# Optimization experiments

Measured on AMD Instinct MI355X. Metric: run time of the kernel, lower is better.

Reference implementation:

```python
import jax, jax.numpy as jnp
import numpy as np

BETA = 0.25


def setup_inputs() -> dict:
    key = jax.random.key(0)
    k1, k2 = jax.random.split(key)
    inputs = jax.random.normal(k1, (32, 4096, 64), dtype=jnp.float32)
    # VarianceScaling(uniform) ~ small-magnitude init; plain normal scaled works for a numeric reference
    codebook = jax.random.normal(k2, (1024, 64), dtype=jnp.float32) * (1.0 / np.sqrt(64.0))
    return {"inputs": inputs, "codebook": codebook}


def reference(inputs, codebook):
    D = codebook.shape[-1]
    flat = jnp.reshape(inputs, (-1, D))                      # [N, D]
    flat_sqr = jnp.sum(flat ** 2, axis=-1, keepdims=True)    # [N, 1]
    code_sqr = jnp.sum(codebook ** 2, axis=-1)[None, :]      # [1, K]
    # full pairwise squared distances [N, K]
    distances = flat_sqr - 2.0 * (flat @ codebook.T) + code_sqr
    encoding_indices = jnp.reshape(jnp.argmin(distances, axis=-1), inputs.shape[:-1])
    quantize = codebook[encoding_indices]                    # gather -> [..., D]
    encoding_loss = jnp.mean((jax.lax.stop_gradient(inputs) - quantize) ** 2)
    commit_loss = jnp.mean((inputs - jax.lax.stop_gradient(quantize)) ** 2)
    loss = encoding_loss + BETA * commit_loss
    # straight-through estimator
    z_q = inputs + jax.lax.stop_gradient(quantize - inputs)
    return loss, z_q, encoding_indices
```

## Files before the change

### kernel.cpp

```cpp
#include <hip/hip_runtime.h>

#define N_ROWS 131072
#define D 64
#define K_CODES 1024
#define RPB 128
#define CH_TILES 4
#define NCHUNK 16

typedef _Float16 f16x8 __attribute__((ext_vector_type(8)));
typedef float    f32x4 __attribute__((ext_vector_type(4)));

#define MFMA16(a, b, c) __builtin_amdgcn_mfma_f32_16x16x32_f16((a), (b), (c), 0, 0, 0)

#define ASYNC_COPY16(gp, lp)                                                  \
    __builtin_amdgcn_global_load_lds(                                         \
        (const __attribute__((address_space(1))) void*)(gp),                  \
        (__attribute__((address_space(3))) void*)(lp), 16, 0, 0)

__global__ __launch_bounds__(256)
void prep_kernel(const float* __restrict__ CB, _Float16* __restrict__ CBf,
                 float* __restrict__ csqr, float* __restrict__ loss) {
    const int b = blockIdx.x, t = threadIdx.x;
    if (b < 64) {
        const int unit = b * 256 + t;
        const int tile = unit >> 8;
        const int f    = (unit >> 6) & 3;
        const int lane = unit & 63;
        const int quad = lane >> 4, lrow = lane & 15;
        const int code = tile * 16 + lrow;
        const int k0   = (f & 1) * 32 + quad * 8;
        const float* src = CB + (size_t)code * D + k0;
        float4 v0 = *(const float4*)(src);
        float4 v1 = *(const float4*)(src + 4);
        float xs[8] = {v0.x, v0.y, v0.z, v0.w, v1.x, v1.y, v1.z, v1.w};
        f16x8 o;
#pragma unroll
        for (int j = 0; j < 8; ++j) {
            _Float16 h = (_Float16)xs[j];
            o[j] = (f < 2) ? h : (_Float16)(xs[j] - (float)h);
        }
        *(f16x8*)(CBf + (size_t)unit * 8) = o;
    } else {
        if (t == 0) *loss = 0.0f;
        for (int k = t; k < K_CODES; k += 256) {
            const float4* p = (const float4*)(CB + (size_t)k * D);
            float s = 0.0f;
#pragma unroll
            for (int i = 0; i < 16; ++i) {
                float4 v = p[i];
                s += v.x * v.x + v.y * v.y + v.z * v.z + v.w * v.w;
            }
            csqr[k] = s;
        }
    }
}

__global__ __launch_bounds__(256, 4)
void argmin_kernel(const float* __restrict__ X,
                   const _Float16* __restrict__ CBf,
                   const float* __restrict__ csqr,
                   const float* __restrict__ CB,
                   float* __restrict__ out) {
    __shared__ __align__(16) _Float16 Bs[2][CH_TILES * 256 * 8];
    __shared__ float LsC[K_CODES];
    __shared__ int   ivfin[RPB];

    const int t    = threadIdx.x;
    const int wave = t >> 6;
    const int lane = t & 63;
    const int lrow = lane & 15;
    const int quad = lane >> 4;
    const int R0   = blockIdx.x * RPB;
    const int Rw   = R0 + wave * 32;

    ((float4*)LsC)[t] = ((const float4*)csqr)[t];

    f16x8 Ah[2][2], Al[2][2];
    float xsq = 0.0f;
#pragma unroll
    for (int mt = 0; mt < 2; ++mt) {
        const float* xr = X + (size_t)(Rw + mt * 16 + lrow) * D;
#pragma unroll
        for (int ks = 0; ks < 2; ++ks) {
            const int k0 = ks * 32 + quad * 8;
            float4 v0 = *(const float4*)(xr + k0);
            float4 v1 = *(const float4*)(xr + k0 + 4);
            float xs[8] = {v0.x, v0.y, v0.z, v0.w, v1.x, v1.y, v1.z, v1.w};
            f16x8 h, l;
#pragma unroll
            for (int j = 0; j < 8; ++j) {
                xsq += xs[j] * xs[j];
                float sv = -2.0f * xs[j];
                _Float16 hh = (_Float16)sv;
                h[j] = hh;
                l[j] = (_Float16)(sv - (float)hh);
            }
            Ah[mt][ks] = h;
            Al[mt][ks] = l;
        }
    }

    float bestd[2][4];
    int   besti[2][4];
#pragma unroll
    for (int mt = 0; mt < 2; ++mt)
#pragma unroll
        for (int r = 0; r < 4; ++r) { bestd[mt][r] = 3.0e38f; besti[mt][r] = 0; }

#define STAGE(c, b)                                                           \
    do {                                                                      \
        const char* gb = (const char*)CBf + (size_t)(c) * 16384               \
                         + wave * 4096 + lane * 16;                           \
        _Float16* lb = &Bs[b][wave * 2048];             \
        ASYNC_COPY16(gb,        lb);                                          \
        ASYNC_COPY16(gb + 1024, lb + 512);                                    \
        ASYNC_COPY16(gb + 2048, lb + 1024);                                   \
        ASYNC_COPY16(gb + 3072, lb + 1536);                                   \
    } while (0)

    STAGE(0, 0);
    __syncthreads();

    for (int c = 0; c < NCHUNK; ++c) {
        const int cb = c & 1;
        if (c + 1 < NCHUNK) STAGE(c + 1, (c + 1) & 1);

#pragma unroll
        for (int tl = 0; tl < CH_TILES; ++tl) {
            const f16x8* bu = (const f16x8*)&Bs[cb][0] + tl * 256 + lane;
            f16x8 Bh0 = bu[0], Bh1 = bu[64], Bl0 = bu[128], Bl1 = bu[192];
            const int   cc = (c * CH_TILES + tl) * 16 + lrow;
            const float cs = LsC[cc];
#pragma unroll
            for (int mt = 0; mt < 2; ++mt) {
                f32x4 acc = {cs, cs, cs, cs};
                acc = MFMA16(Ah[mt][0], Bh0, acc);
                acc = MFMA16(Ah[mt][1], Bh1, acc);
                acc = MFMA16(Al[mt][0], Bh0, acc);
                acc = MFMA16(Al[mt][1], Bh1, acc);
                acc = MFMA16(Ah[mt][0], Bl0, acc);
                acc = MFMA16(Ah[mt][1], Bl1, acc);
#pragma unroll
                for (int r = 0; r < 4; ++r) {
                    bool lt = acc[r] < bestd[mt][r];
                    bestd[mt][r] = lt ? acc[r] : bestd[mt][r];
                    besti[mt][r] = lt ? cc : besti[mt][r];
                }
            }
        }
        __syncthreads();
    }

    const float scale = 1.25f / (float)((size_t)N_ROWS * D);

    float ssum = 0.0f;
#pragma unroll
    for (int mt = 0; mt < 2; ++mt) {
#pragma unroll
        for (int r = 0; r < 4; ++r) {
            float dv = bestd[mt][r];
            int   iv = besti[mt][r];
#pragma unroll
            for (int m = 1; m < 16; m <<= 1) {
                float od = __shfl_xor(dv, m, 64);
                int   oi = __shfl_xor(iv, m, 64);
                if (od < dv || (od == dv && oi < iv)) { dv = od; iv = oi; }
            }
            if (lrow == 0) {
                int rl = wave * 32 + mt * 16 + quad * 4 + r;
                ivfin[rl] = iv;
                out[1 + (size_t)N_ROWS * D + R0 + rl] = (float)iv;
                ssum += dv;
            }
        }
    }
    ssum += __shfl_xor(ssum, 16, 64);
    ssum += __shfl_xor(ssum, 32, 64);
#pragma unroll
    for (int m = 1; m < 64; m <<= 1) xsq += __shfl_xor(xsq, m, 64);
    if (lane == 0) atomicAdd(out, (ssum + xsq) * scale);
    __syncthreads();

    float* p = out + 1 + (size_t)R0 * D;
#pragma unroll
    for (int i = 0; i < 8; ++i) {
        int q = i * 256 + t;
        int j = 4 * q + 3;
        if (q < 2047) {
            float v[4];
#pragma unroll
            for (int e = 0; e < 4; ++e) {
                int jj = j + e;
                v[e] = CB[(size_t)ivfin[jj >> 6] * D + (jj & 63)];
            }
            *(float4*)(p + j) = make_float4(v[0], v[1], v[2], v[3]);
        } else if (q == 2047) {
            p[8191] = CB[(size_t)ivfin[RPB - 1] * D + 63];
        }
    }
    if (t == 0) {
        const float* c0 = CB + (size_t)ivfin[0] * D;
        p[0] = c0[0];
        p[1] = c0[1];
        p[2] = c0[2];
    }
}

extern "C" void kernel_launch(void* const* d_in, const int* in_sizes, int n_in,
                              void* d_out, int out_size, void* d_ws,
                              size_t ws_size, hipStream_t stream) {
    const float* X  = (const float*)d_in[0];
    const float* CB = (const float*)d_in[1];

    float*    csqr = (float*)d_ws;
    _Float16* CBf  = (_Float16*)((char*)d_ws + 4096);

    hipLaunchKernelGGL(prep_kernel, dim3(65), dim3(256), 0, stream,
                       CB, CBf, csqr, (float*)d_out);
    hipLaunchKernelGGL(argmin_kernel, dim3(N_ROWS / RPB), dim3(256), 0, stream,
                       X, CBf, csqr, CB, (float*)d_out);
}
```

Baseline: 176.9 us.

## Split codebook across grid dimension with 64-bit atomicMin argmin merge

The codebook is split into four 256-code slices along a second grid dimension. Each 512-thread block loads its whole slice into LDS once instead of streaming double-buffered chunks, and reduces its local argmin into a global 64-bit key (ordered distance bits plus index) with atomicMin. A new finish kernel decodes the keys, writes the indices, adds the distance sum into the loss and gathers the quantized rows. This raises parallelism and removes the per-chunk barriers. In exchange it adds a third launch, global atomics, and recomputes the fp32-to-fp16 split of X in every slice.

```diff
diff --git a/kernel.cpp b/kernel.cpp
--- a/kernel.cpp
+++ b/kernel.cpp
@@ -3,23 +3,16 @@
 #define N_ROWS 131072
 #define D 64
 #define K_CODES 1024
-#define RPB 128
-#define CH_TILES 4
-#define NCHUNK 16
 
 typedef _Float16 f16x8 __attribute__((ext_vector_type(8)));
 typedef float    f32x4 __attribute__((ext_vector_type(4)));
 
 #define MFMA16(a, b, c) __builtin_amdgcn_mfma_f32_16x16x32_f16((a), (b), (c), 0, 0, 0)
 
-#define ASYNC_COPY16(gp, lp)                                                  \
-    __builtin_amdgcn_global_load_lds(                                         \
-        (const __attribute__((address_space(1))) void*)(gp),                  \
-        (__attribute__((address_space(3))) void*)(lp), 16, 0, 0)
-
 __global__ __launch_bounds__(256)
 void prep_kernel(const float* __restrict__ CB, _Float16* __restrict__ CBf,
-                 float* __restrict__ csqr, float* __restrict__ loss) {
+                 float* __restrict__ csqr, unsigned long long* __restrict__ keys,
+                 float* __restrict__ loss) {
     const int b = blockIdx.x, t = threadIdx.x;
     if (b < 64) {
         const int unit = b * 256 + t;
@@ -40,7 +33,7 @@
             o[j] = (f < 2) ? h : (_Float16)(xs[j] - (float)h);
         }
         *(f16x8*)(CBf + (size_t)unit * 8) = o;
-    } else {
+    } else if (b == 64) {
         if (t == 0) *loss = 0.0f;
         for (int k = t; k < K_CODES; k += 256) {
             const float4* p = (const float4*)(CB + (size_t)k * D);
@@ -52,28 +45,36 @@
             }
             csqr[k] = s;
         }
-    }
-}
-
-__global__ __launch_bounds__(256, 4)
+    } else {
+        keys[(size_t)(b - 65) * 256 + t] = 0xFFFFFFFFFFFFFFFFULL;
+    }
+}
+
+__global__ __launch_bounds__(512, 4)
 void argmin_kernel(const float* __restrict__ X,
                    const _Float16* __restrict__ CBf,
                    const float* __restrict__ csqr,
-                   const float* __restrict__ CB,
+                   unsigned long long* __restrict__ keys,
                    float* __restrict__ out) {
-    __shared__ __align__(16) _Float16 Bs[2][CH_TILES * 256 * 8];
-    __shared__ float LsC[K_CODES];
-    __shared__ int   ivfin[RPB];
+    __shared__ __align__(16) _Float16 Bs[16 * 256 * 8];
+    __shared__ float LsC[256];
 
     const int t    = threadIdx.x;
     const int wave = t >> 6;
     const int lane = t & 63;
     const int lrow = lane & 15;
     const int quad = lane >> 4;
-    const int R0   = blockIdx.x * RPB;
+    const int cq   = blockIdx.y;
+    const int R0   = blockIdx.x * 256;
     const int Rw   = R0 + wave * 32;
 
-    ((float4*)LsC)[t] = ((const float4*)csqr)[t];
+    if (t < 64) ((float4*)LsC)[t] = ((const float4*)(csqr + cq * 256))[t];
+    {
+        const f16x8* src = (const f16x8*)CBf + (size_t)cq * 4096;
+        f16x8* dst = (f16x8*)Bs;
+#pragma unroll
+        for (int i = 0; i < 8; ++i) dst[i * 512 + t] = src[i * 512 + t];
+    }
 
     f16x8 Ah[2][2], Al[2][2];
     float xsq = 0.0f;
@@ -99,6 +100,7 @@
             Al[mt][ks] = l;
         }
     }
+    __syncthreads();
 
     float bestd[2][4];
     int   besti[2][4];
@@ -107,53 +109,38 @@
 #pragma unroll
         for (int r = 0; r < 4; ++r) { bestd[mt][r] = 3.0e38f; besti[mt][r] = 0; }
 
-#define STAGE(c, b)                                                           \
-    do {                                                                      \
-        const char* gb = (const char*)CBf + (size_t)(c) * 16384               \
-                         + wave * 4096 + lane * 16;                           \
-        _Float16* lb = &Bs[b][wave * 2048];             \
-        ASYNC_COPY16(gb,        lb);                                          \
-        ASYNC_COPY16(gb + 1024, lb + 512);                                    \
-        ASYNC_COPY16(gb + 2048, lb + 1024);                                   \
-        ASYNC_COPY16(gb + 3072, lb + 1536);                                   \
-    } while (0)
-
-    STAGE(0, 0);
-    __syncthreads();
-
-    for (int c = 0; c < NCHUNK; ++c) {
-        const int cb = c & 1;
-        if (c + 1 < NCHUNK) STAGE(c + 1, (c + 1) & 1);
-
-#pragma unroll
-        for (int tl = 0; tl < CH_TILES; ++tl) {
-            const f16x8* bu = (const f16x8*)&Bs[cb][0] + tl * 256 + lane;
-            f16x8 Bh0 = bu[0], Bh1 = bu[64], Bl0 = bu[128], Bl1 = bu[192];
-            const int   cc = (c * CH_TILES + tl) * 16 + lrow;
-            const float cs = LsC[cc];
-#pragma unroll
-            for (int mt = 0; mt < 2; ++mt) {
-                f32x4 acc = {cs, cs, cs, cs};
-                acc = MFMA16(Ah[mt][0], Bh0, acc);
-                acc = MFMA16(Ah[mt][1], Bh1, acc);
-                acc = MFMA16(Al[mt][0], Bh0, acc);
-                acc = MFMA16(Al[mt][1], Bh1, acc);
-                acc = MFMA16(Ah[mt][0], Bl0, acc);
-                acc = MFMA16(Ah[mt][1], Bl1, acc);
-#pragma unroll
-                for (int r = 0; r < 4; ++r) {
-                    bool lt = acc[r] < bestd[mt][r];
-                    bestd[mt][r] = lt ? acc[r] : bestd[mt][r];
-                    besti[mt][r] = lt ? cc : besti[mt][r];
-                }
-            }
-        }
-        __syncthreads();
-    }
-
-    const float scale = 1.25f / (float)((size_t)N_ROWS * D);
-
-    float ssum = 0.0f;
+#pragma unroll 2
+    for (int tl = 0; tl < 16; ++tl) {
+        const f16x8* bu = (const f16x8*)Bs + tl * 256 + lane;
+        f16x8 Bh0 = bu[0], Bh1 = bu[64], Bl0 = bu[128], Bl1 = bu[192];
+        const int   cc = cq * 256 + tl * 16 + lrow;
+        const float cs = LsC[tl * 16 + lrow];
+#pragma unroll
+        for (int mt = 0; mt < 2; ++mt) {
+            f32x4 acc = {cs, cs, cs, cs};
+            acc = MFMA16(Ah[mt][0], Bh0, acc);
+            acc = MFMA16(Ah[mt][1], Bh1, acc);
+            acc = MFMA16(Al[mt][0], Bh0, acc);
+            acc = MFMA16(Al[mt][1], Bh1, acc);
+            acc = MFMA16(Ah[mt][0], Bl0, acc);
+            acc = MFMA16(Ah[mt][1], Bl1, acc);
+#pragma unroll
+            for (int r = 0; r < 4; ++r) {
+                bool lt = acc[r] < bestd[mt][r];
+                bestd[mt][r] = lt ? acc[r] : bestd[mt][r];
+                besti[mt][r] = lt ? cc : besti[mt][r];
+            }
+        }
+    }
+
+    if (cq == 0) {
+        float s = xsq;
+#pragma unroll
+        for (int m = 1; m < 64; m <<= 1) s += __shfl_xor(s, m, 64);
+        if (lane == 0)
+            atomicAdd(out, s * (1.25f / (float)((size_t)N_ROWS * D)));
+    }
+
 #pragma unroll
     for (int mt = 0; mt < 2; ++mt) {
 #pragma unroll
@@ -167,26 +154,48 @@
                 if (od < dv || (od == dv && oi < iv)) { dv = od; iv = oi; }
             }
             if (lrow == 0) {
-                int rl = wave * 32 + mt * 16 + quad * 4 + r;
-                ivfin[rl] = iv;
-                out[1 + (size_t)N_ROWS * D + R0 + rl] = (float)iv;
-                ssum += dv;
-            }
-        }
-    }
-    ssum += __shfl_xor(ssum, 16, 64);
-    ssum += __shfl_xor(ssum, 32, 64);
-#pragma unroll
-    for (int m = 1; m < 64; m <<= 1) xsq += __shfl_xor(xsq, m, 64);
-    if (lane == 0) atomicAdd(out, (ssum + xsq) * scale);
+                int row = Rw + mt * 16 + quad * 4 + r;
+                unsigned ub = __float_as_uint(dv);
+                ub = (ub & 0x80000000u) ? ~ub : (ub | 0x80000000u);
+                unsigned long long key =
+                    ((unsigned long long)ub << 32) | (unsigned)iv;
+                atomicMin(&keys[row], key);
+            }
+        }
+    }
+}
+
+__global__ __launch_bounds__(256)
+void finish_kernel(const float* __restrict__ CB,
+                   const unsigned long long* __restrict__ keys,
+                   float* __restrict__ out) {
+    __shared__ int   ivfin[256];
+    __shared__ float red[256];
+    const int t  = threadIdx.x;
+    const int R0 = blockIdx.x * 256;
+
+    unsigned long long key = keys[R0 + t];
+    int      iv = (int)(key & 0xFFFFFFFFu);
+    unsigned ud = (unsigned)(key >> 32);
+    unsigned bb = (ud & 0x80000000u) ? (ud ^ 0x80000000u) : ~ud;
+    float    dv = __uint_as_float(bb);
+    ivfin[t] = iv;
+    out[1 + (size_t)N_ROWS * D + R0 + t] = (float)iv;
+    red[t] = dv;
     __syncthreads();
+    for (int s = 128; s > 0; s >>= 1) {
+        if (t < s) red[t] += red[t + s];
+        __syncthreads();
+    }
+    if (t == 0)
+        atomicAdd(out, red[0] * (1.25f / (float)((size_t)N_ROWS * D)));
 
     float* p = out + 1 + (size_t)R0 * D;
 #pragma unroll
-    for (int i = 0; i < 8; ++i) {
+    for (int i = 0; i < 16; ++i) {
         int q = i * 256 + t;
         int j = 4 * q + 3;
-        if (q < 2047) {
+        if (q < 4095) {
             float v[4];
 #pragma unroll
             for (int e = 0; e < 4; ++e) {
@@ -194,8 +203,8 @@
                 v[e] = CB[(size_t)ivfin[jj >> 6] * D + (jj & 63)];
             }
             *(float4*)(p + j) = make_float4(v[0], v[1], v[2], v[3]);
-        } else if (q == 2047) {
-            p[8191] = CB[(size_t)ivfin[RPB - 1] * D + 63];
+        } else {
+            p[16383] = CB[(size_t)ivfin[255] * D + 63];
         }
     }
     if (t == 0) {
@@ -214,9 +223,13 @@
 
     float*    csqr = (float*)d_ws;
     _Float16* CBf  = (_Float16*)((char*)d_ws + 4096);
-
-    hipLaunchKernelGGL(prep_kernel, dim3(65), dim3(256), 0, stream,
-                       CB, CBf, csqr, (float*)d_out);
-    hipLaunchKernelGGL(argmin_kernel, dim3(N_ROWS / RPB), dim3(256), 0, stream,
-                       X, CBf, csqr, CB, (float*)d_out);
-}
+    unsigned long long* keys =
+        (unsigned long long*)((char*)d_ws + 4096 + 262144);
+
+    hipLaunchKernelGGL(prep_kernel, dim3(65 + 512), dim3(256), 0, stream,
+                       CB, CBf, csqr, keys, (float*)d_out);
+    hipLaunchKernelGGL(argmin_kernel, dim3(512, 4), dim3(512), 0, stream,
+                       X, CBf, csqr, keys, (float*)d_out);
+    hipLaunchKernelGGL(finish_kernel, dim3(512), dim3(256), 0, stream,
+                       CB, keys, (float*)d_out);
+}
```

Result: slower. 201.3 us (+13.7%).
